# Kernel optimization log

Measured on AMD Instinct MI355X. Metric: run time of the kernel, lower is better.

Reference implementation:

```python
import jax, jax.numpy as jnp
import numpy as np

NUM_HEAD = 2


def setup_inputs() -> dict:
    key = jax.random.key(0)
    k1, k2, k3 = jax.random.split(key, 3)
    B, G, L, C = 16, 64, 256, 128
    x = jax.random.normal(k1, (B, G, L, C), dtype=jnp.float32)
    W_qkv = jax.random.normal(k2, (3 * C, C), dtype=jnp.float32) * (C ** -0.5)
    b_qkv = jax.random.normal(k3, (3 * C,), dtype=jnp.float32) * 0.02
    return {"x": x, "W_qkv": W_qkv, "b_qkv": b_qkv}


def reference(x, W_qkv, b_qkv):
    B, G, L, C = x.shape
    H = NUM_HEAD
    c = C // H
    scale = C ** 0.5  # NOTE: source scales by sqrt(full channel), not sqrt(head dim)
    # qkv projection: [b, g, l, 3C]
    qkv = jnp.einsum('bglc,dc->bgld', x, W_qkv) + b_qkv
    # split (d h c): d outermost, then heads, then per-head channels
    qkv = qkv.reshape(B, G, L, 3, H, c).transpose(3, 0, 1, 4, 2, 5)  # [3, b, g, h, l, c]
    q, k, v = qkv[0], qkv[1], qkv[2]
    score = jnp.einsum('bghlc,bghmc->bghlm', q, k) / scale  # [b, g, h, l, l]
    score = jax.nn.softmax(score, axis=-1)
    out = jnp.einsum('bghlm,bghmc->bghlc', score, v)  # [b, g, h, l, c]
    # 'b g h l c -> b g l (h c)'
    out = out.transpose(0, 1, 3, 2, 4).reshape(B, G, L, C)
    return out
```

## Files before the change

### kernel.cpp

```cpp
#include <hip/hip_runtime.h>
#include <hip/hip_bf16.h>
#include <cstdint>
#include <cstddef>


typedef __attribute__((ext_vector_type(8))) short v8s;
typedef __attribute__((ext_vector_type(4))) float v4f;
typedef __attribute__((ext_vector_type(4))) unsigned short v4u;

#define MFMA16(a, b, c) __builtin_amdgcn_mfma_f32_16x16x32_bf16((a), (b), (c), 0, 0, 0)

constexpr int LL = 256;
constexpr int CC = 128;
constexpr int CH = 64;
constexpr int KS_BYTES = 256 * 128;
constexpr int VT_BYTES = 64 * 512;

__device__ __forceinline__ unsigned short f2bf(float f) {
    union { __hip_bfloat16 b; unsigned short u; } cv;
    cv.b = __float2bfloat16(f);
    return cv.u;
}

__device__ __forceinline__ v8s load8_f32_bf16(const float* __restrict__ p) {
    float4 a = *reinterpret_cast<const float4*>(p);
    float4 b = *reinterpret_cast<const float4*>(p + 4);
    v8s r;
    r[0] = (short)f2bf(a.x); r[1] = (short)f2bf(a.y);
    r[2] = (short)f2bf(a.z); r[3] = (short)f2bf(a.w);
    r[4] = (short)f2bf(b.x); r[5] = (short)f2bf(b.y);
    r[6] = (short)f2bf(b.z); r[7] = (short)f2bf(b.w);
    return r;
}

__device__ __forceinline__ int swz128(int row, int byte_in_row) {
    return row * 128 + (byte_in_row ^ ((row & 7) << 4));
}
__device__ __forceinline__ int swz512(int row, int byte_in_row) {
    return row * 512 + (byte_in_row ^ ((row & 7) << 4));
}

__global__ __launch_bounds__(256) void wconv_kernel(
    const float* __restrict__ W, unsigned short* __restrict__ Wb)
{
    int i = blockIdx.x * 256 + threadIdx.x;
    float4 v = reinterpret_cast<const float4*>(W)[i];
    const float s = (i < 4096) ? 0.08838834764831845f : 1.0f;
    v4u o;
    o[0] = f2bf(v.x * s); o[1] = f2bf(v.y * s); o[2] = f2bf(v.z * s); o[3] = f2bf(v.w * s);
    reinterpret_cast<v4u*>(Wb)[i] = o;
}

__global__ __launch_bounds__(512, 4) void lmsa_kernel(
    const float* __restrict__ x, const unsigned short* __restrict__ Wb,
    const float* __restrict__ bias, float* __restrict__ out)
{
    __shared__ char smem[KS_BYTES + VT_BYTES];
    char* KsB = smem;
    char* VtB = smem + KS_BYTES;

    const int bgh  = blockIdx.x;
    const int bg   = bgh >> 1;
    const int h    = bgh & 1;
    const int tid  = threadIdx.x;
    const int wave = tid >> 6;
    const int lane = tid & 63;
    const int m_   = lane & 15;
    const int g    = lane >> 4;
    const int pm   = 8 * (m_ >> 2) + (m_ & 3);

    const float* xB = x + (size_t)bg * (LL * CC);
    const size_t obase0 = (size_t)bg * (LL * CC);

    const unsigned short* Wq = Wb + (0 * CC + h * CH) * CC;
    const unsigned short* Wk = Wb + (1 * CC + h * CH) * CC;
    const unsigned short* Wv = Wb + (2 * CC + h * CH) * CC;
    const float* bq = bias + 0 * CC + h * CH;
    const float* bk = bias + 1 * CC + h * CH;
    const float* bv = bias + 2 * CC + h * CH;

    const float qscale = 0.08838834764831845f;

    float bkr[4];
    #pragma unroll
    for (int nt = 0; nt < 4; ++nt) bkr[nt] = bk[16 * nt + m_];

    v8s af[2][4];
    #pragma unroll
    for (int i = 0; i < 2; ++i)
        #pragma unroll
        for (int ks = 0; ks < 4; ++ks)
            af[i][ks] = load8_f32_bf16(xB + (32 * wave + 16 * i + m_) * CC + 32 * ks + 8 * g);

    #pragma unroll 2
    for (int nt = 0; nt < 4; ++nt) {
        v8s bf[4];
        #pragma unroll
        for (int ks = 0; ks < 4; ++ks)
            bf[ks] = *reinterpret_cast<const v8s*>(Wk + (16 * nt + m_) * CC + 32 * ks + 8 * g);
        const int kcol = (32 * (nt >> 1) + 4 * (nt & 1) + pm) << 1;
        #pragma unroll
        for (int i = 0; i < 2; ++i) {
            v4f acc = {0.f, 0.f, 0.f, 0.f};
            #pragma unroll
            for (int ks = 0; ks < 4; ++ks) acc = MFMA16(af[i][ks], bf[ks], acc);
            #pragma unroll
            for (int r = 0; r < 4; ++r)
                *(unsigned short*)(KsB + swz128(16 * (2 * wave + i) + 4 * g + r, kcol)) =
                    f2bf(acc[r] + bkr[nt]);
        }
    }

    v8s qf[2][2];
    #pragma unroll
    for (int i = 0; i < 2; ++i) {
        v4f qacc[4];
        #pragma unroll
        for (int mtc = 0; mtc < 4; ++mtc) {
            v4f acc = {0.f, 0.f, 0.f, 0.f};
            #pragma unroll
            for (int ks = 0; ks < 4; ++ks) {
                v8s wf = *reinterpret_cast<const v8s*>(Wq + (16 * mtc + m_) * CC + 32 * ks + 8 * g);
                acc = MFMA16(wf, af[i][ks], acc);
            }
            #pragma unroll
            for (int r = 0; r < 4; ++r)
                qacc[mtc][r] = acc[r] + bq[16 * mtc + 4 * g + r] * qscale;
        }
        #pragma unroll
        for (int ks = 0; ks < 2; ++ks)
            #pragma unroll
            for (int j = 0; j < 8; ++j)
                qf[i][ks][j] = (short)f2bf(qacc[2 * ks + (j >> 2)][j & 3]);
    }

    #pragma unroll 2
    for (int mtc = 0; mtc < 4; ++mtc) {
        v8s wf[4];
        #pragma unroll
        for (int ks = 0; ks < 4; ++ks)
            wf[ks] = *reinterpret_cast<const v8s*>(Wv + (16 * mtc + m_) * CC + 32 * ks + 8 * g);
        v4f bvv = *reinterpret_cast<const v4f*>(bv + 16 * mtc + 4 * g);
        #pragma unroll
        for (int i = 0; i < 2; ++i) {
            const int mt = 2 * wave + i;
            const int vcol = (32 * (mt >> 1) + 4 * (mt & 1) + pm) << 1;
            v4f acc = {0.f, 0.f, 0.f, 0.f};
            #pragma unroll
            for (int ks = 0; ks < 4; ++ks) acc = MFMA16(wf[ks], af[i][ks], acc);
            #pragma unroll
            for (int r = 0; r < 4; ++r)
                *(unsigned short*)(VtB + swz512(16 * mtc + 4 * g + r, vcol)) =
                    f2bf(acc[r] + bvv[r]);
        }
    }

    __syncthreads();

    #pragma unroll
    for (int chk = 0; chk < 2; ++chk) {
        v4f o[4];
        #pragma unroll
        for (int nt = 0; nt < 4; ++nt) o[nt] = v4f{0.f, 0.f, 0.f, 0.f};
        float sm = 0.f;

        #pragma unroll 2
        for (int c2 = 0; c2 < 8; ++c2) {
            v4f s0 = {0.f, 0.f, 0.f, 0.f}, s1 = {0.f, 0.f, 0.f, 0.f};
            #pragma unroll
            for (int ks = 0; ks < 2; ++ks) {
                v8s kf0 = *reinterpret_cast<const v8s*>(
                    KsB + swz128(32 * c2 + m_, (32 * ks + 8 * g) << 1));
                s0 = MFMA16(kf0, qf[chk][ks], s0);
            }
            #pragma unroll
            for (int ks = 0; ks < 2; ++ks) {
                v8s kf1 = *reinterpret_cast<const v8s*>(
                    KsB + swz128(32 * c2 + 16 + m_, (32 * ks + 8 * g) << 1));
                s1 = MFMA16(kf1, qf[chk][ks], s1);
            }

            v8s pf;
            #pragma unroll
            for (int j = 0; j < 4; ++j) {
                float p = __expf(s0[j]); sm += p; pf[j] = (short)f2bf(p);
            }
            #pragma unroll
            for (int j = 0; j < 4; ++j) {
                float p = __expf(s1[j]); sm += p; pf[4 + j] = (short)f2bf(p);
            }

            #pragma unroll
            for (int nt = 0; nt < 4; ++nt) {
                v8s vf = *reinterpret_cast<const v8s*>(
                    VtB + swz512(16 * nt + m_, 64 * c2 + 16 * g));
                o[nt] = MFMA16(pf, vf, o[nt]);
            }
        }

        sm += __shfl_xor(sm, 16, 64);
        sm += __shfl_xor(sm, 32, 64);
        float inv[4];
        #pragma unroll
        for (int r = 0; r < 4; ++r) inv[r] = 1.0f / __shfl(sm, 4 * g + r, 64);

        const int rowb = 32 * wave + 16 * chk;
        #pragma unroll
        for (int nt = 0; nt < 4; ++nt)
            #pragma unroll
            for (int r = 0; r < 4; ++r)
                out[obase0 + (size_t)(rowb + 4 * g + r) * CC + h * CH + 16 * nt + m_] =
                    o[nt][r] * inv[r];
    }
}

extern "C" void kernel_launch(void* const* d_in, const int* in_sizes, int n_in,
                              void* d_out, int out_size, void* d_ws, size_t ws_size,
                              hipStream_t stream) {
    (void)in_sizes; (void)n_in; (void)ws_size; (void)out_size;
    const float* x = (const float*)d_in[0];
    const float* W = (const float*)d_in[1];
    const float* b = (const float*)d_in[2];
    float* out = (float*)d_out;
    unsigned short* Wb = (unsigned short*)d_ws;

    wconv_kernel<<<dim3(48), dim3(256), 0, stream>>>(W, Wb);
    lmsa_kernel<<<dim3(2048), dim3(512), 0, stream>>>(x, Wb, b, out);
}
```

Before: 174.5 us.

## Process keys/values in two halves to halve LDS and raise occupancy

Splits the K/V projection and attention into two 128-row halves, reusing a half-size LDS buffer for K and V^T. Each wave now owns 16 query rows from each half, and the outputs and softmax sums accumulate across both halves. Halving shared memory allows the launch bound to rise from 4 to 6 blocks per SM, and s_setprio is added around the PV MFMAs. The cost is an extra barrier, a second pass over K/V weights, and reloading the second half of x between the passes.

```diff
diff --git a/kernel.cpp b/kernel.cpp
--- a/kernel.cpp
+++ b/kernel.cpp
@@ -13,8 +13,8 @@
 constexpr int LL = 256;
 constexpr int CC = 128;
 constexpr int CH = 64;
-constexpr int KS_BYTES = 256 * 128;
-constexpr int VT_BYTES = 64 * 512;
+constexpr int KS_BYTES = 128 * 128;
+constexpr int VT_BYTES = 64 * 256;
 
 __device__ __forceinline__ unsigned short f2bf(float f) {
     union { __hip_bfloat16 b; unsigned short u; } cv;
@@ -36,8 +36,8 @@
 __device__ __forceinline__ int swz128(int row, int byte_in_row) {
     return row * 128 + (byte_in_row ^ ((row & 7) << 4));
 }
-__device__ __forceinline__ int swz512(int row, int byte_in_row) {
-    return row * 512 + (byte_in_row ^ ((row & 7) << 4));
+__device__ __forceinline__ int swz256(int row, int byte_in_row) {
+    return row * 256 + (byte_in_row ^ ((row & 7) << 4));
 }
 
 __global__ __launch_bounds__(256) void wconv_kernel(
@@ -51,7 +51,7 @@
     reinterpret_cast<v4u*>(Wb)[i] = o;
 }
 
-__global__ __launch_bounds__(512, 4) void lmsa_kernel(
+__global__ __launch_bounds__(512, 6) void lmsa_kernel(
     const float* __restrict__ x, const unsigned short* __restrict__ Wb,
     const float* __restrict__ bias, float* __restrict__ out)
 {
@@ -85,35 +85,17 @@
     #pragma unroll
     for (int nt = 0; nt < 4; ++nt) bkr[nt] = bk[16 * nt + m_];
 
-    v8s af[2][4];
-    #pragma unroll
-    for (int i = 0; i < 2; ++i)
-        #pragma unroll
-        for (int ks = 0; ks < 4; ++ks)
-            af[i][ks] = load8_f32_bf16(xB + (32 * wave + 16 * i + m_) * CC + 32 * ks + 8 * g);
-
-    #pragma unroll 2
-    for (int nt = 0; nt < 4; ++nt) {
-        v8s bf[4];
-        #pragma unroll
-        for (int ks = 0; ks < 4; ++ks)
-            bf[ks] = *reinterpret_cast<const v8s*>(Wk + (16 * nt + m_) * CC + 32 * ks + 8 * g);
-        const int kcol = (32 * (nt >> 1) + 4 * (nt & 1) + pm) << 1;
-        #pragma unroll
-        for (int i = 0; i < 2; ++i) {
-            v4f acc = {0.f, 0.f, 0.f, 0.f};
-            #pragma unroll
-            for (int ks = 0; ks < 4; ++ks) acc = MFMA16(af[i][ks], bf[ks], acc);
-            #pragma unroll
-            for (int r = 0; r < 4; ++r)
-                *(unsigned short*)(KsB + swz128(16 * (2 * wave + i) + 4 * g + r, kcol)) =
-                    f2bf(acc[r] + bkr[nt]);
-        }
-    }
+    v8s af0[4], af1[4];
+    #pragma unroll
+    for (int ks = 0; ks < 4; ++ks)
+        af0[ks] = load8_f32_bf16(xB + (16 * wave + m_) * CC + 32 * ks + 8 * g);
+    #pragma unroll
+    for (int ks = 0; ks < 4; ++ks)
+        af1[ks] = load8_f32_bf16(xB + (128 + 16 * wave + m_) * CC + 32 * ks + 8 * g);
 
     v8s qf[2][2];
     #pragma unroll
-    for (int i = 0; i < 2; ++i) {
+    for (int qg = 0; qg < 2; ++qg) {
         v4f qacc[4];
         #pragma unroll
         for (int mtc = 0; mtc < 4; ++mtc) {
@@ -121,7 +103,7 @@
             #pragma unroll
             for (int ks = 0; ks < 4; ++ks) {
                 v8s wf = *reinterpret_cast<const v8s*>(Wq + (16 * mtc + m_) * CC + 32 * ks + 8 * g);
-                acc = MFMA16(wf, af[i][ks], acc);
+                acc = MFMA16(wf, qg ? af1[ks] : af0[ks], acc);
             }
             #pragma unroll
             for (int r = 0; r < 4; ++r)
@@ -131,86 +113,120 @@
         for (int ks = 0; ks < 2; ++ks)
             #pragma unroll
             for (int j = 0; j < 8; ++j)
-                qf[i][ks][j] = (short)f2bf(qacc[2 * ks + (j >> 2)][j & 3]);
+                qf[qg][ks][j] = (short)f2bf(qacc[2 * ks + (j >> 2)][j & 3]);
     }
 
-    #pragma unroll 2
-    for (int mtc = 0; mtc < 4; ++mtc) {
-        v8s wf[4];
-        #pragma unroll
-        for (int ks = 0; ks < 4; ++ks)
-            wf[ks] = *reinterpret_cast<const v8s*>(Wv + (16 * mtc + m_) * CC + 32 * ks + 8 * g);
-        v4f bvv = *reinterpret_cast<const v4f*>(bv + 16 * mtc + 4 * g);
-        #pragma unroll
-        for (int i = 0; i < 2; ++i) {
-            const int mt = 2 * wave + i;
-            const int vcol = (32 * (mt >> 1) + 4 * (mt & 1) + pm) << 1;
+    v4f o[2][4];
+    #pragma unroll
+    for (int qg = 0; qg < 2; ++qg)
+        #pragma unroll
+        for (int nt = 0; nt < 4; ++nt) o[qg][nt] = v4f{0.f, 0.f, 0.f, 0.f};
+    float sm[2] = {0.f, 0.f};
+
+    #pragma unroll
+    for (int hf = 0; hf < 2; ++hf) {
+        #pragma unroll 2
+        for (int nt = 0; nt < 4; ++nt) {
+            v8s bf[4];
+            #pragma unroll
+            for (int ks = 0; ks < 4; ++ks)
+                bf[ks] = *reinterpret_cast<const v8s*>(Wk + (16 * nt + m_) * CC + 32 * ks + 8 * g);
+            const int kcol = (32 * (nt >> 1) + 4 * (nt & 1) + pm) << 1;
             v4f acc = {0.f, 0.f, 0.f, 0.f};
             #pragma unroll
-            for (int ks = 0; ks < 4; ++ks) acc = MFMA16(wf[ks], af[i][ks], acc);
+            for (int ks = 0; ks < 4; ++ks)
+                acc = MFMA16(hf ? af1[ks] : af0[ks], bf[ks], acc);
             #pragma unroll
             for (int r = 0; r < 4; ++r)
-                *(unsigned short*)(VtB + swz512(16 * mtc + 4 * g + r, vcol)) =
-                    f2bf(acc[r] + bvv[r]);
+                *(unsigned short*)(KsB + swz128(16 * wave + 4 * g + r, kcol)) =
+                    f2bf(acc[r] + bkr[nt]);
+        }
+
+        {
+            const int vcol = (32 * (wave >> 1) + 4 * (wave & 1) + pm) << 1;
+            #pragma unroll 2
+            for (int mtc = 0; mtc < 4; ++mtc) {
+                v8s wf[4];
+                #pragma unroll
+                for (int ks = 0; ks < 4; ++ks)
+                    wf[ks] = *reinterpret_cast<const v8s*>(Wv + (16 * mtc + m_) * CC + 32 * ks + 8 * g);
+                v4f bvv = *reinterpret_cast<const v4f*>(bv + 16 * mtc + 4 * g);
+                v4f acc = {0.f, 0.f, 0.f, 0.f};
+                #pragma unroll
+                for (int ks = 0; ks < 4; ++ks)
+                    acc = MFMA16(wf[ks], hf ? af1[ks] : af0[ks], acc);
+                #pragma unroll
+                for (int r = 0; r < 4; ++r)
+                    *(unsigned short*)(VtB + swz256(16 * mtc + 4 * g + r, vcol)) =
+                        f2bf(acc[r] + bvv[r]);
+            }
+        }
+
+        __syncthreads();
+
+        #pragma unroll
+        for (int qg = 0; qg < 2; ++qg) {
+            #pragma unroll 2
+            for (int c2 = 0; c2 < 4; ++c2) {
+                v4f s0 = {0.f, 0.f, 0.f, 0.f}, s1 = {0.f, 0.f, 0.f, 0.f};
+                #pragma unroll
+                for (int ks = 0; ks < 2; ++ks) {
+                    v8s kf0 = *reinterpret_cast<const v8s*>(
+                        KsB + swz128(32 * c2 + m_, (32 * ks + 8 * g) << 1));
+                    s0 = MFMA16(kf0, qf[qg][ks], s0);
+                }
+                #pragma unroll
+                for (int ks = 0; ks < 2; ++ks) {
+                    v8s kf1 = *reinterpret_cast<const v8s*>(
+                        KsB + swz128(32 * c2 + 16 + m_, (32 * ks + 8 * g) << 1));
+                    s1 = MFMA16(kf1, qf[qg][ks], s1);
+                }
+
+                v8s pf;
+                #pragma unroll
+                for (int j = 0; j < 4; ++j) {
+                    float p = __expf(s0[j]); sm[qg] += p; pf[j] = (short)f2bf(p);
+                }
+                #pragma unroll
+                for (int j = 0; j < 4; ++j) {
+                    float p = __expf(s1[j]); sm[qg] += p; pf[4 + j] = (short)f2bf(p);
+                }
+
+                __builtin_amdgcn_s_setprio(1);
+                #pragma unroll
+                for (int nt = 0; nt < 4; ++nt) {
+                    v8s vf = *reinterpret_cast<const v8s*>(
+                        VtB + swz256(16 * nt + m_, 64 * c2 + 16 * g));
+                    o[qg][nt] = MFMA16(pf, vf, o[qg][nt]);
+                }
+                __builtin_amdgcn_s_setprio(0);
+            }
+        }
+
+        if (hf == 0) {
+            #pragma unroll
+            for (int ks = 0; ks < 4; ++ks)
+                af1[ks] = load8_f32_bf16(xB + (128 + 16 * wave + m_) * CC + 32 * ks + 8 * g);
+            __syncthreads();
         }
     }
 
-    __syncthreads();
-
-    #pragma unroll
-    for (int chk = 0; chk < 2; ++chk) {
-        v4f o[4];
-        #pragma unroll
-        for (int nt = 0; nt < 4; ++nt) o[nt] = v4f{0.f, 0.f, 0.f, 0.f};
-        float sm = 0.f;
-
-        #pragma unroll 2
-        for (int c2 = 0; c2 < 8; ++c2) {
-            v4f s0 = {0.f, 0.f, 0.f, 0.f}, s1 = {0.f, 0.f, 0.f, 0.f};
-            #pragma unroll
-            for (int ks = 0; ks < 2; ++ks) {
-                v8s kf0 = *reinterpret_cast<const v8s*>(
-                    KsB + swz128(32 * c2 + m_, (32 * ks + 8 * g) << 1));
-                s0 = MFMA16(kf0, qf[chk][ks], s0);
-            }
-            #pragma unroll
-            for (int ks = 0; ks < 2; ++ks) {
-                v8s kf1 = *reinterpret_cast<const v8s*>(
-                    KsB + swz128(32 * c2 + 16 + m_, (32 * ks + 8 * g) << 1));
-                s1 = MFMA16(kf1, qf[chk][ks], s1);
-            }
-
-            v8s pf;
-            #pragma unroll
-            for (int j = 0; j < 4; ++j) {
-                float p = __expf(s0[j]); sm += p; pf[j] = (short)f2bf(p);
-            }
-            #pragma unroll
-            for (int j = 0; j < 4; ++j) {
-                float p = __expf(s1[j]); sm += p; pf[4 + j] = (short)f2bf(p);
-            }
-
-            #pragma unroll
-            for (int nt = 0; nt < 4; ++nt) {
-                v8s vf = *reinterpret_cast<const v8s*>(
-                    VtB + swz512(16 * nt + m_, 64 * c2 + 16 * g));
-                o[nt] = MFMA16(pf, vf, o[nt]);
-            }
-        }
-
-        sm += __shfl_xor(sm, 16, 64);
-        sm += __shfl_xor(sm, 32, 64);
+    #pragma unroll
+    for (int qg = 0; qg < 2; ++qg) {
+        float s = sm[qg];
+        s += __shfl_xor(s, 16, 64);
+        s += __shfl_xor(s, 32, 64);
         float inv[4];
         #pragma unroll
-        for (int r = 0; r < 4; ++r) inv[r] = 1.0f / __shfl(sm, 4 * g + r, 64);
-
-        const int rowb = 32 * wave + 16 * chk;
+        for (int r = 0; r < 4; ++r) inv[r] = 1.0f / __shfl(s, 4 * g + r, 64);
+
+        const int rowb = 128 * qg + 16 * wave;
         #pragma unroll
         for (int nt = 0; nt < 4; ++nt)
             #pragma unroll
             for (int r = 0; r < 4; ++r)
                 out[obase0 + (size_t)(rowb + 4 * g + r) * CC + h * CH + 16 * nt + m_] =
-                    o[nt][r] * inv[r];
+                    o[qg][nt][r] * inv[r];
     }
 }
 
```

Result: slower. 336.6 us (+92.9%).

## Fuse query chunk loops to reuse K/V LDS fragments across both chunks

Applied to the files above, without the earlier changes.

Swaps the loop order in the attention phase so each K and V fragment loaded from LDS serves both 16-row query chunks, halving LDS reads in the main loop. It also wraps the PV MFMAs in s_setprio to raise wave priority around matrix issue. The cost is more live registers (two sets of accumulators plus the buffered K/V fragments), which could pressure occupancy at launch bounds (512,4).

```diff
diff --git a/kernel.cpp b/kernel.cpp
--- a/kernel.cpp
+++ b/kernel.cpp
@@ -157,52 +157,63 @@
 
     __syncthreads();
 
+    v4f o[2][4];
+    #pragma unroll
+    for (int chk = 0; chk < 2; ++chk)
+        #pragma unroll
+        for (int nt = 0; nt < 4; ++nt) o[chk][nt] = v4f{0.f, 0.f, 0.f, 0.f};
+    float sm[2] = {0.f, 0.f};
+
+    #pragma unroll 2
+    for (int c2 = 0; c2 < 8; ++c2) {
+        v8s kf0[2], kf1[2], vf[4];
+        #pragma unroll
+        for (int ks = 0; ks < 2; ++ks)
+            kf0[ks] = *reinterpret_cast<const v8s*>(
+                KsB + swz128(32 * c2 + m_, (32 * ks + 8 * g) << 1));
+        #pragma unroll
+        for (int ks = 0; ks < 2; ++ks)
+            kf1[ks] = *reinterpret_cast<const v8s*>(
+                KsB + swz128(32 * c2 + 16 + m_, (32 * ks + 8 * g) << 1));
+        #pragma unroll
+        for (int nt = 0; nt < 4; ++nt)
+            vf[nt] = *reinterpret_cast<const v8s*>(
+                VtB + swz512(16 * nt + m_, 64 * c2 + 16 * g));
+
+        #pragma unroll
+        for (int chk = 0; chk < 2; ++chk) {
+            v4f s0 = {0.f, 0.f, 0.f, 0.f}, s1 = {0.f, 0.f, 0.f, 0.f};
+            #pragma unroll
+            for (int ks = 0; ks < 2; ++ks) s0 = MFMA16(kf0[ks], qf[chk][ks], s0);
+            #pragma unroll
+            for (int ks = 0; ks < 2; ++ks) s1 = MFMA16(kf1[ks], qf[chk][ks], s1);
+
+            v8s pf;
+            #pragma unroll
+            for (int j = 0; j < 4; ++j) {
+                float p = __expf(s0[j]); sm[chk] += p; pf[j] = (short)f2bf(p);
+            }
+            #pragma unroll
+            for (int j = 0; j < 4; ++j) {
+                float p = __expf(s1[j]); sm[chk] += p; pf[4 + j] = (short)f2bf(p);
+            }
+
+            __builtin_amdgcn_s_setprio(1);
+            #pragma unroll
+            for (int nt = 0; nt < 4; ++nt)
+                o[chk][nt] = MFMA16(pf, vf[nt], o[chk][nt]);
+            __builtin_amdgcn_s_setprio(0);
+        }
+    }
+
     #pragma unroll
     for (int chk = 0; chk < 2; ++chk) {
-        v4f o[4];
-        #pragma unroll
-        for (int nt = 0; nt < 4; ++nt) o[nt] = v4f{0.f, 0.f, 0.f, 0.f};
-        float sm = 0.f;
-
-        #pragma unroll 2
-        for (int c2 = 0; c2 < 8; ++c2) {
-            v4f s0 = {0.f, 0.f, 0.f, 0.f}, s1 = {0.f, 0.f, 0.f, 0.f};
-            #pragma unroll
-            for (int ks = 0; ks < 2; ++ks) {
-                v8s kf0 = *reinterpret_cast<const v8s*>(
-                    KsB + swz128(32 * c2 + m_, (32 * ks + 8 * g) << 1));
-                s0 = MFMA16(kf0, qf[chk][ks], s0);
-            }
-            #pragma unroll
-            for (int ks = 0; ks < 2; ++ks) {
-                v8s kf1 = *reinterpret_cast<const v8s*>(
-                    KsB + swz128(32 * c2 + 16 + m_, (32 * ks + 8 * g) << 1));
-                s1 = MFMA16(kf1, qf[chk][ks], s1);
-            }
-
-            v8s pf;
-            #pragma unroll
-            for (int j = 0; j < 4; ++j) {
-                float p = __expf(s0[j]); sm += p; pf[j] = (short)f2bf(p);
-            }
-            #pragma unroll
-            for (int j = 0; j < 4; ++j) {
-                float p = __expf(s1[j]); sm += p; pf[4 + j] = (short)f2bf(p);
-            }
-
-            #pragma unroll
-            for (int nt = 0; nt < 4; ++nt) {
-                v8s vf = *reinterpret_cast<const v8s*>(
-                    VtB + swz512(16 * nt + m_, 64 * c2 + 16 * g));
-                o[nt] = MFMA16(pf, vf, o[nt]);
-            }
-        }
-
-        sm += __shfl_xor(sm, 16, 64);
-        sm += __shfl_xor(sm, 32, 64);
+        float s = sm[chk];
+        s += __shfl_xor(s, 16, 64);
+        s += __shfl_xor(s, 32, 64);
         float inv[4];
         #pragma unroll
-        for (int r = 0; r < 4; ++r) inv[r] = 1.0f / __shfl(sm, 4 * g + r, 64);
+        for (int r = 0; r < 4; ++r) inv[r] = 1.0f / __shfl(s, 4 * g + r, 64);
 
         const int rowb = 32 * wave + 16 * chk;
         #pragma unroll
@@ -210,7 +221,7 @@
             #pragma unroll
             for (int r = 0; r < 4; ++r)
                 out[obase0 + (size_t)(rowb + 4 * g + r) * CC + h * CH + 16 * nt + m_] =
-                    o[nt][r] * inv[r];
+                    o[chk][nt][r] * inv[r];
     }
 }
 
```

Result: faster. 156.6 us (-10.3%).

## Switch attention kernel to 32x32x16 MFMA tiles with permlane32 swap repacking

Applied to the files above, without the earlier changes.

Rewrites the QKV projection and attention loops to use the 32x32x16 bf16 MFMA instead of 16x16x32, with each wave handling a 32-row query tile in a single pass. Score-to-operand repacking uses packed bf16 conversion plus permlane32_swap, which keeps P in registers without going through LDS. The row-sum reduction drops to a single shuffle, and the output is written with vectorized float4 stores. It also raises wave priority around the PV MFMAs. The larger accumulators increase register pressure, which may lower occupancy.

```diff
diff --git a/kernel.cpp b/kernel.cpp
--- a/kernel.cpp
+++ b/kernel.cpp
@@ -6,9 +6,11 @@
 
 typedef __attribute__((ext_vector_type(8))) short v8s;
 typedef __attribute__((ext_vector_type(4))) float v4f;
+typedef __attribute__((ext_vector_type(16))) float v16f;
 typedef __attribute__((ext_vector_type(4))) unsigned short v4u;
-
-#define MFMA16(a, b, c) __builtin_amdgcn_mfma_f32_16x16x32_bf16((a), (b), (c), 0, 0, 0)
+typedef __attribute__((ext_vector_type(4))) unsigned int v4i;
+
+#define MFMA32(a, b, c) __builtin_amdgcn_mfma_f32_32x32x16_bf16((a), (b), (c), 0, 0, 0)
 
 constexpr int LL = 256;
 constexpr int CC = 128;
@@ -22,15 +24,21 @@
     return cv.u;
 }
 
+__device__ __forceinline__ unsigned int pk2(float lo, float hi) {
+    union { __hip_bfloat162 b; unsigned int u; } cv;
+    cv.b = __float22bfloat162_rn(float2{lo, hi});
+    return cv.u;
+}
+
 __device__ __forceinline__ v8s load8_f32_bf16(const float* __restrict__ p) {
     float4 a = *reinterpret_cast<const float4*>(p);
     float4 b = *reinterpret_cast<const float4*>(p + 4);
-    v8s r;
-    r[0] = (short)f2bf(a.x); r[1] = (short)f2bf(a.y);
-    r[2] = (short)f2bf(a.z); r[3] = (short)f2bf(a.w);
-    r[4] = (short)f2bf(b.x); r[5] = (short)f2bf(b.y);
-    r[6] = (short)f2bf(b.z); r[7] = (short)f2bf(b.w);
-    return r;
+    union { v4i i; v8s s; } u;
+    u.i[0] = pk2(a.x, a.y);
+    u.i[1] = pk2(a.z, a.w);
+    u.i[2] = pk2(b.x, b.y);
+    u.i[3] = pk2(b.z, b.w);
+    return u.s;
 }
 
 __device__ __forceinline__ int swz128(int row, int byte_in_row) {
@@ -38,6 +46,20 @@
 }
 __device__ __forceinline__ int swz512(int row, int byte_in_row) {
     return row * 512 + (byte_in_row ^ ((row & 7) << 4));
+}
+
+__device__ __forceinline__ v8s pack_swap8(float a0, float a1, float a2, float a3,
+                                          float a4, float a5, float a6, float a7) {
+    int d0 = (int)pk2(a0, a1), d1 = (int)pk2(a2, a3);
+    int d2 = (int)pk2(a4, a5), d3 = (int)pk2(a6, a7);
+    auto r02 = __builtin_amdgcn_permlane32_swap(d0, d2, false, false);
+    auto r13 = __builtin_amdgcn_permlane32_swap(d1, d3, false, false);
+    union { v4i i4; v8s s8; } u;
+    u.i4[0] = (unsigned)r02[0];
+    u.i4[1] = (unsigned)r13[0];
+    u.i4[2] = (unsigned)r02[1];
+    u.i4[3] = (unsigned)r13[1];
+    return u.s8;
 }
 
 __global__ __launch_bounds__(256) void wconv_kernel(
@@ -65,9 +87,8 @@
     const int tid  = threadIdx.x;
     const int wave = tid >> 6;
     const int lane = tid & 63;
-    const int m_   = lane & 15;
-    const int g    = lane >> 4;
-    const int pm   = 8 * (m_ >> 2) + (m_ & 3);
+    const int q31  = lane & 31;
+    const int hh   = lane >> 5;
 
     const float* xB = x + (size_t)bg * (LL * CC);
     const size_t obase0 = (size_t)bg * (LL * CC);
@@ -81,136 +102,122 @@
 
     const float qscale = 0.08838834764831845f;
 
-    float bkr[4];
-    #pragma unroll
-    for (int nt = 0; nt < 4; ++nt) bkr[nt] = bk[16 * nt + m_];
-
-    v8s af[2][4];
-    #pragma unroll
-    for (int i = 0; i < 2; ++i)
-        #pragma unroll
-        for (int ks = 0; ks < 4; ++ks)
-            af[i][ks] = load8_f32_bf16(xB + (32 * wave + 16 * i + m_) * CC + 32 * ks + 8 * g);
+    v8s af[8];
+    #pragma unroll
+    for (int ks = 0; ks < 8; ++ks)
+        af[ks] = load8_f32_bf16(xB + (32 * wave + q31) * CC + 16 * ks + 8 * hh);
+
+    #pragma unroll
+    for (int t = 0; t < 2; ++t) {
+        v16f acc = {0,0,0,0, 0,0,0,0, 0,0,0,0, 0,0,0,0};
+        #pragma unroll
+        for (int ks = 0; ks < 8; ++ks) {
+            v8s wkf = *reinterpret_cast<const v8s*>(Wk + (32 * t + q31) * CC + 16 * ks + 8 * hh);
+            acc = MFMA32(af[ks], wkf, acc);
+        }
+        const float bkv = bk[32 * t + q31];
+        const int cb = (32 * t + q31) << 1;
+        #pragma unroll
+        for (int r = 0; r < 16; ++r) {
+            const int key = 32 * wave + (r & 3) + 8 * (r >> 2) + 4 * hh;
+            *(unsigned short*)(KsB + swz128(key, cb)) = f2bf(acc[r] + bkv);
+        }
+    }
+
+    #pragma unroll
+    for (int t = 0; t < 2; ++t) {
+        v16f acc = {0,0,0,0, 0,0,0,0, 0,0,0,0, 0,0,0,0};
+        #pragma unroll
+        for (int ks = 0; ks < 8; ++ks) {
+            v8s wvf = *reinterpret_cast<const v8s*>(Wv + (32 * t + q31) * CC + 16 * ks + 8 * hh);
+            acc = MFMA32(wvf, af[ks], acc);
+        }
+        v4f bv4[4];
+        #pragma unroll
+        for (int b = 0; b < 4; ++b)
+            bv4[b] = *reinterpret_cast<const v4f*>(bv + 32 * t + 8 * b + 4 * hh);
+        const int kb = (32 * wave + q31) << 1;
+        #pragma unroll
+        for (int r = 0; r < 16; ++r) {
+            const int cc = 32 * t + (r & 3) + 8 * (r >> 2) + 4 * hh;
+            *(unsigned short*)(VtB + swz512(cc, kb)) = f2bf(acc[r] + bv4[r >> 2][r & 3]);
+        }
+    }
+
+    v8s qB[4];
+    #pragma unroll
+    for (int t = 0; t < 2; ++t) {
+        v16f acc = {0,0,0,0, 0,0,0,0, 0,0,0,0, 0,0,0,0};
+        #pragma unroll
+        for (int ks = 0; ks < 8; ++ks) {
+            v8s wqf = *reinterpret_cast<const v8s*>(Wq + (32 * t + q31) * CC + 16 * ks + 8 * hh);
+            acc = MFMA32(wqf, af[ks], acc);
+        }
+        v4f bq4[4];
+        #pragma unroll
+        for (int b = 0; b < 4; ++b)
+            bq4[b] = *reinterpret_cast<const v4f*>(bq + 32 * t + 8 * b + 4 * hh);
+        float qv[16];
+        #pragma unroll
+        for (int r = 0; r < 16; ++r)
+            qv[r] = acc[r] + bq4[r >> 2][r & 3] * qscale;
+        qB[2 * t + 0] = pack_swap8(qv[0], qv[1], qv[2], qv[3], qv[4], qv[5], qv[6], qv[7]);
+        qB[2 * t + 1] = pack_swap8(qv[8], qv[9], qv[10], qv[11], qv[12], qv[13], qv[14], qv[15]);
+    }
+
+    __syncthreads();
+
+    v16f o0 = {0,0,0,0, 0,0,0,0, 0,0,0,0, 0,0,0,0};
+    v16f o1 = {0,0,0,0, 0,0,0,0, 0,0,0,0, 0,0,0,0};
+    float sm = 0.f;
 
     #pragma unroll 2
-    for (int nt = 0; nt < 4; ++nt) {
-        v8s bf[4];
-        #pragma unroll
-        for (int ks = 0; ks < 4; ++ks)
-            bf[ks] = *reinterpret_cast<const v8s*>(Wk + (16 * nt + m_) * CC + 32 * ks + 8 * g);
-        const int kcol = (32 * (nt >> 1) + 4 * (nt & 1) + pm) << 1;
-        #pragma unroll
-        for (int i = 0; i < 2; ++i) {
-            v4f acc = {0.f, 0.f, 0.f, 0.f};
-            #pragma unroll
-            for (int ks = 0; ks < 4; ++ks) acc = MFMA16(af[i][ks], bf[ks], acc);
-            #pragma unroll
-            for (int r = 0; r < 4; ++r)
-                *(unsigned short*)(KsB + swz128(16 * (2 * wave + i) + 4 * g + r, kcol)) =
-                    f2bf(acc[r] + bkr[nt]);
-        }
-    }
-
-    v8s qf[2][2];
-    #pragma unroll
-    for (int i = 0; i < 2; ++i) {
-        v4f qacc[4];
-        #pragma unroll
-        for (int mtc = 0; mtc < 4; ++mtc) {
-            v4f acc = {0.f, 0.f, 0.f, 0.f};
-            #pragma unroll
-            for (int ks = 0; ks < 4; ++ks) {
-                v8s wf = *reinterpret_cast<const v8s*>(Wq + (16 * mtc + m_) * CC + 32 * ks + 8 * g);
-                acc = MFMA16(wf, af[i][ks], acc);
-            }
-            #pragma unroll
-            for (int r = 0; r < 4; ++r)
-                qacc[mtc][r] = acc[r] + bq[16 * mtc + 4 * g + r] * qscale;
-        }
-        #pragma unroll
-        for (int ks = 0; ks < 2; ++ks)
-            #pragma unroll
-            for (int j = 0; j < 8; ++j)
-                qf[i][ks][j] = (short)f2bf(qacc[2 * ks + (j >> 2)][j & 3]);
-    }
-
-    #pragma unroll 2
-    for (int mtc = 0; mtc < 4; ++mtc) {
-        v8s wf[4];
-        #pragma unroll
-        for (int ks = 0; ks < 4; ++ks)
-            wf[ks] = *reinterpret_cast<const v8s*>(Wv + (16 * mtc + m_) * CC + 32 * ks + 8 * g);
-        v4f bvv = *reinterpret_cast<const v4f*>(bv + 16 * mtc + 4 * g);
-        #pragma unroll
-        for (int i = 0; i < 2; ++i) {
-            const int mt = 2 * wave + i;
-            const int vcol = (32 * (mt >> 1) + 4 * (mt & 1) + pm) << 1;
-            v4f acc = {0.f, 0.f, 0.f, 0.f};
-            #pragma unroll
-            for (int ks = 0; ks < 4; ++ks) acc = MFMA16(wf[ks], af[i][ks], acc);
-            #pragma unroll
-            for (int r = 0; r < 4; ++r)
-                *(unsigned short*)(VtB + swz512(16 * mtc + 4 * g + r, vcol)) =
-                    f2bf(acc[r] + bvv[r]);
-        }
-    }
-
-    __syncthreads();
-
-    #pragma unroll
-    for (int chk = 0; chk < 2; ++chk) {
-        v4f o[4];
-        #pragma unroll
-        for (int nt = 0; nt < 4; ++nt) o[nt] = v4f{0.f, 0.f, 0.f, 0.f};
-        float sm = 0.f;
-
-        #pragma unroll 2
-        for (int c2 = 0; c2 < 8; ++c2) {
-            v4f s0 = {0.f, 0.f, 0.f, 0.f}, s1 = {0.f, 0.f, 0.f, 0.f};
-            #pragma unroll
-            for (int ks = 0; ks < 2; ++ks) {
-                v8s kf0 = *reinterpret_cast<const v8s*>(
-                    KsB + swz128(32 * c2 + m_, (32 * ks + 8 * g) << 1));
-                s0 = MFMA16(kf0, qf[chk][ks], s0);
-            }
-            #pragma unroll
-            for (int ks = 0; ks < 2; ++ks) {
-                v8s kf1 = *reinterpret_cast<const v8s*>(
-                    KsB + swz128(32 * c2 + 16 + m_, (32 * ks + 8 * g) << 1));
-                s1 = MFMA16(kf1, qf[chk][ks], s1);
-            }
-
-            v8s pf;
-            #pragma unroll
-            for (int j = 0; j < 4; ++j) {
-                float p = __expf(s0[j]); sm += p; pf[j] = (short)f2bf(p);
-            }
-            #pragma unroll
-            for (int j = 0; j < 4; ++j) {
-                float p = __expf(s1[j]); sm += p; pf[4 + j] = (short)f2bf(p);
-            }
-
-            #pragma unroll
-            for (int nt = 0; nt < 4; ++nt) {
-                v8s vf = *reinterpret_cast<const v8s*>(
-                    VtB + swz512(16 * nt + m_, 64 * c2 + 16 * g));
-                o[nt] = MFMA16(pf, vf, o[nt]);
-            }
-        }
-
-        sm += __shfl_xor(sm, 16, 64);
-        sm += __shfl_xor(sm, 32, 64);
-        float inv[4];
-        #pragma unroll
-        for (int r = 0; r < 4; ++r) inv[r] = 1.0f / __shfl(sm, 4 * g + r, 64);
-
-        const int rowb = 32 * wave + 16 * chk;
-        #pragma unroll
-        for (int nt = 0; nt < 4; ++nt)
-            #pragma unroll
-            for (int r = 0; r < 4; ++r)
-                out[obase0 + (size_t)(rowb + 4 * g + r) * CC + h * CH + 16 * nt + m_] =
-                    o[nt][r] * inv[r];
+    for (int c2 = 0; c2 < 8; ++c2) {
+        v8s ksf[4], vtf[4];
+        #pragma unroll
+        for (int s = 0; s < 4; ++s)
+            ksf[s] = *reinterpret_cast<const v8s*>(
+                KsB + swz128(32 * c2 + q31, 32 * s + 16 * hh));
+        vtf[0] = *reinterpret_cast<const v8s*>(VtB + swz512(q31,      64 * c2 +  0 + 16 * hh));
+        vtf[1] = *reinterpret_cast<const v8s*>(VtB + swz512(q31,      64 * c2 + 32 + 16 * hh));
+        vtf[2] = *reinterpret_cast<const v8s*>(VtB + swz512(q31 + 32, 64 * c2 +  0 + 16 * hh));
+        vtf[3] = *reinterpret_cast<const v8s*>(VtB + swz512(q31 + 32, 64 * c2 + 32 + 16 * hh));
+
+        v16f sa = {0,0,0,0, 0,0,0,0, 0,0,0,0, 0,0,0,0};
+        #pragma unroll
+        for (int s = 0; s < 4; ++s) sa = MFMA32(ksf[s], qB[s], sa);
+
+        float p[16];
+        #pragma unroll
+        for (int r = 0; r < 16; ++r) p[r] = __expf(sa[r]);
+        #pragma unroll
+        for (int r = 0; r < 16; ++r) sm += p[r];
+
+        const v8s pB0 = pack_swap8(p[0], p[1], p[2], p[3], p[4], p[5], p[6], p[7]);
+        const v8s pB1 = pack_swap8(p[8], p[9], p[10], p[11], p[12], p[13], p[14], p[15]);
+
+        __builtin_amdgcn_s_setprio(1);
+        o0 = MFMA32(vtf[0], pB0, o0);
+        o0 = MFMA32(vtf[1], pB1, o0);
+        o1 = MFMA32(vtf[2], pB0, o1);
+        o1 = MFMA32(vtf[3], pB1, o1);
+        __builtin_amdgcn_s_setprio(0);
+    }
+
+    sm += __shfl_xor(sm, 32, 64);
+    const float inv = 1.0f / sm;
+
+    float* op = out + obase0 + (size_t)(32 * wave + q31) * CC + h * CH;
+    #pragma unroll
+    for (int b = 0; b < 4; ++b) {
+        v4f v0, v1;
+        #pragma unroll
+        for (int a = 0; a < 4; ++a) {
+            v0[a] = o0[4 * b + a] * inv;
+            v1[a] = o1[4 * b + a] * inv;
+        }
+        *reinterpret_cast<v4f*>(op +  0 + 8 * b + 4 * hh) = v0;
+        *reinterpret_cast<v4f*>(op + 32 + 8 * b + 4 * hh) = v1;
     }
 }
 
```

Result: faster. 159.1 us (-8.8%).
